# Optimization experiments

Measured on AMD Instinct MI355X. Metric: run time of the kernel, lower is better.

Reference implementation:

```python
import jax, jax.numpy as jnp
import numpy as np

DIM_X, DIM_Z, D_MODEL, N_HEADS, BATCH = 512, 256, 256, 8, 32


def sinusoidal_pe(seq_len, d_model):
    # standard sinusoidal table, rows indexed by position
    pos = np.arange(seq_len)[:, None].astype(np.float32)
    div = np.exp(np.arange(0, d_model, 2).astype(np.float32) * (-np.log(10000.0) / d_model))
    pe = np.zeros((seq_len, d_model), dtype=np.float32)
    pe[:, 0::2] = np.sin(pos * div)
    pe[:, 1::2] = np.cos(pos * div)
    return jnp.asarray(pe)


def setup_inputs() -> dict:
    key = jax.random.key(0)
    ks = jax.random.split(key, 5)
    state = jax.random.normal(ks[0], (BATCH, D_MODEL, DIM_X), dtype=jnp.float32)
    obs = jax.random.normal(ks[1], (BATCH, D_MODEL, DIM_Z), dtype=jnp.float32)
    Qp = jax.random.uniform(ks[2], (DIM_X, D_MODEL), dtype=jnp.float32)  # torch.rand init
    Wq = jax.random.normal(ks[3], (D_MODEL, D_MODEL), dtype=jnp.float32) / np.sqrt(D_MODEL)
    Wk = jax.random.normal(ks[4], (D_MODEL, D_MODEL), dtype=jnp.float32) / np.sqrt(D_MODEL)
    bq = jnp.zeros((D_MODEL,), dtype=jnp.float32)
    bk = jnp.zeros((D_MODEL,), dtype=jnp.float32)
    return {"state": state, "obs": obs, "Qp": Qp, "Wq": Wq, "bq": bq, "Wk": Wk, "bk": bk}


def reference(state, obs, Qp, Wq, bq, Wk, bk):
    bs, en, dim_x = state.shape
    dim_z = obs.shape[2]
    d_model = Qp.shape[1]
    h = N_HEADS
    hd = d_model // h
    S = dim_x + dim_z

    # mean-center over the ensemble axis
    A = state - jnp.mean(state, axis=1, keepdims=True)   # [bs, en, dim_x]
    Y = obs - jnp.mean(obs, axis=1, keepdims=True)       # [bs, en, dim_z]
    A = jnp.transpose(A, (2, 0, 1))                      # [dim_x, bs, en]
    Y = jnp.transpose(Y, (2, 0, 1))                      # [dim_z, bs, en]

    # positional encoding: batch_first=True quirk -> PE indexed along axis 1 (the bs axis)
    pe = sinusoidal_pe(bs, d_model)[None, :, :]          # [1, bs, d_model]
    query = Qp[:, None, :] + pe                          # [dim_x, bs, d_model] (broadcast of repeat)
    xy = jnp.concatenate([A, Y], axis=0) + pe            # [S, bs, d_model]

    # multi-head attention weights (V / out-proj do not affect returned quantities)
    q = (query @ Wq.T + bq).reshape(dim_x, bs, h, hd)
    k = (xy @ Wk.T + bk).reshape(S, bs, h, hd)
    scores = jnp.einsum('lbhd,sbhd->bhls', q, k) / np.sqrt(hd)  # [bs, h, dim_x, S]

    # fixed structured mask: eye(dim_x) | bottom-padded eye(dim_z)
    p1 = jnp.eye(dim_x, dtype=bool)
    p2 = jnp.concatenate([jnp.zeros((dim_x - dim_z, dim_z), dtype=bool),
                          jnp.eye(dim_z, dtype=bool)], axis=0)
    allow = jnp.concatenate([p1, p2], axis=1)            # [dim_x, S]
    scores = jnp.where(allow[None, None], scores, -jnp.inf)
    atten = jnp.mean(jax.nn.softmax(scores, axis=-1), axis=1)  # average over heads -> [bs, dim_x, S]

    # weighted merge of the ORIGINAL (uncentered) state/obs
    merge = jnp.concatenate([jnp.transpose(state, (0, 2, 1)),
                             jnp.transpose(obs, (0, 2, 1))], axis=1)  # [bs, S, en]
    new_state = jnp.einsum('bls,bse->ble', atten, merge)              # [bs, dim_x, en]
    new_state = jnp.transpose(new_state, (0, 2, 1))                   # [bs, en, dim_x]
    return new_state, atten
```

## Files before the change

### kernel.cpp

```cpp
#include <hip/hip_runtime.h>
#include <stdint.h>
#include <math.h>


#define WS_P    0
#define WS_QWT  8192
#define WS_PQ   73728
#define WS_U    81920
#define WS_V    606208
#define WS_QPT  671744
#define WS_WQT  737280

__global__ void __launch_bounds__(256)
k_tr(const float* __restrict__ Qp, const float* __restrict__ Wq,
     float* __restrict__ ws) {
  __shared__ float tile[32][33];
  int bid = blockIdx.x, t = threadIdx.x;
  const float* src; float* dst; int ti;
  if (bid < 64) { src = Qp + 65536; dst = ws + WS_QPT; ti = bid; }
  else          { src = Wq;         dst = ws + WS_WQT; ti = bid - 64; }
  int tr = ti >> 3, tc = ti & 7;
  int c = t & 31, r0 = t >> 5;
  #pragma unroll
  for (int k = 0; k < 4; ++k) {
    int r = r0 + (k << 3);
    tile[r][c] = src[(size_t)(tr * 32 + r) * 256 + tc * 32 + c];
  }
  __syncthreads();
  #pragma unroll
  for (int k = 0; k < 4; ++k) {
    int r = r0 + (k << 3);
    dst[(size_t)(tc * 32 + r) * 256 + tr * 32 + c] = tile[c][r];
  }
}

__global__ void __launch_bounds__(256)
k_pro(const float* __restrict__ Wq, float* __restrict__ ws) {
  int bid = blockIdx.x, t = threadIdx.x;
  __shared__ float lvec[256];
  const float* __restrict__ GT; float* dst;
  if (bid < 256) {
    int d = bid;
    lvec[t] = Wq[(size_t)d * 256 + t];
    GT = ws + WS_QPT; dst = ws + WS_QWT + d * 256;
  } else {
    int b = bid - 256;
    int k2 = t & ~1;
    float div = expf((float)k2 * (-9.210340371976184f / 256.f));
    float a = (float)b * div;
    lvec[t] = (t & 1) ? cosf(a) : sinf(a);
    GT = ws + WS_WQT; dst = ws + WS_PQ + b * 256;
  }
  __syncthreads();
  float acc = 0.f;
  #pragma unroll 8
  for (int e = 0; e < 256; ++e)
    acc += lvec[e] * GT[(e << 8) + t];
  dst[t] = acc;
}

__global__ void __launch_bounds__(256)
k_uv(const float* __restrict__ Wk, const float* __restrict__ bq,
     float* __restrict__ ws) {
  int bid = blockIdx.x, t = threadIdx.x;
  if (bid < 2048) {
    int h = bid >> 8, e = bid & 255;
    float acc = 0.f;
#pragma unroll 8
    for (int dd = 0; dd < 32; ++dd) {
      int d = h * 32 + dd;
      acc += ws[WS_QWT + d * 256 + t] * Wk[(size_t)d * 256 + e];
    }
    ws[WS_U + ((h << 8) + e) * 256 + t] = acc;
  } else {
    int idx = bid - 2048, b = idx >> 3, h = idx & 7;
    float acc = 0.f;
#pragma unroll 8
    for (int dd = 0; dd < 32; ++dd) {
      int d = h * 32 + dd;
      acc += (ws[WS_PQ + b * 256 + d] + bq[d]) * Wk[(size_t)d * 256 + t];
    }
    ws[WS_V + ((b << 3) + h) * 256 + t] = acc;
  }
}

__global__ void __launch_bounds__(256)
k_delta(const float* __restrict__ state, const float* __restrict__ obs,
        float* __restrict__ ws) {
  int b = blockIdx.x >> 3, jt = (blockIdx.x & 7) << 5;
  int t = threadIdx.x;
  __shared__ float Xs[256][33];
  __shared__ float Vs[2048];
  __shared__ float pd[8][8][32];
  __shared__ float pw[8][8][32];
  __shared__ float px[8][32];
  {
    int es = t >> 3, jq = t & 7;
    const float* sp = state + (size_t)b * 131072 + 256 + jt + (jq << 2);
    const float* op = obs   + (size_t)b * 65536  + jt + (jq << 2);
    #pragma unroll
    for (int k = 0; k < 8; ++k) {
      int e = es + (k << 5);
      float4 s4 = *(const float4*)(sp + (size_t)e * 512);
      float4 o4 = *(const float4*)(op + (size_t)e * 256);
      float* xr = &Xs[e][jq << 2];
      xr[0] = s4.x - o4.x; xr[1] = s4.y - o4.y;
      xr[2] = s4.z - o4.z; xr[3] = s4.w - o4.w;
    }
    for (int i = t; i < 2048; i += 256) Vs[i] = ws[WS_V + (b << 11) + i];
  }
  __syncthreads();
  int j = t & 31, eg = t >> 5, e0 = eg << 5;
  {
    float ax = 0.f;
    #pragma unroll
    for (int ei = 0; ei < 32; ++ei) ax += Xs[e0 + ei][j];
    px[eg][j] = ax;
  }
  const float* __restrict__ Ub = ws + WS_U + jt + j;
  #pragma unroll
  for (int h = 0; h < 8; ++h) {
    float dacc = 0.f, wacc = 0.f;
    const float* __restrict__ Uh = Ub + (h << 16) + (e0 << 8);
    const float* __restrict__ Vh = Vs + (h << 8) + e0;
    #pragma unroll 16
    for (int ei = 0; ei < 32; ++ei) {
      float w = Uh[ei << 8] + Vh[ei];
      dacc += Xs[e0 + ei][j] * w;
      wacc += w;
    }
    pd[eg][h][j] = dacc;
    pw[eg][h][j] = wacc;
  }
  __syncthreads();
  int h2 = t >> 5, j2 = t & 31;
  float D = 0.f, W = 0.f, X = 0.f;
  #pragma unroll
  for (int g = 0; g < 8; ++g) {
    D += pd[g][h2][j2];
    W += pw[g][h2][j2];
    X += px[g][j2];
  }
  float delta = D - X * (1.f / 256.f) * W;
  float sig = 1.f / (1.f + __expf(-delta * 0.17677669529663687f));
  __syncthreads();
  px[h2][j2] = sig;
  __syncthreads();
  if (t < 32) {
    float acc = 0.f;
    #pragma unroll
    for (int h = 0; h < 8; ++h) acc += px[h][t];
    ws[WS_P + (b << 8) + jt + t] = acc;
  }
}

__global__ void __launch_bounds__(256)
k_out(const float* __restrict__ state, const float* __restrict__ obs,
      const float* __restrict__ ws, float* __restrict__ out) {
  int bid = blockIdx.x, t = threadIdx.x;
  if (bid < 4096) {
    int row = (bid << 1) | (t >> 7);
    int tt = t & 127;
    int b = row >> 8;
    float4 sv = ((const float4*)(state + (size_t)row * 512))[tt];
    float4* wrow = (float4*)(out + (size_t)row * 512);
    if (tt < 64) {
      wrow[tt] = sv;
    } else {
      float4 ov = ((const float4*)(obs + (size_t)row * 256))[tt - 64];
      float4 p4 = ((const float4*)(ws + WS_P + b * 256))[tt - 64];
      p4.x *= 0.125f; p4.y *= 0.125f; p4.z *= 0.125f; p4.w *= 0.125f;
      float4 r;
      r.x = p4.x * sv.x + (1.f - p4.x) * ov.x;
      r.y = p4.y * sv.y + (1.f - p4.y) * ov.y;
      r.z = p4.z * sv.z + (1.f - p4.z) * ov.z;
      r.w = p4.w * sv.w + (1.f - p4.w) * ov.w;
      wrow[tt] = r;
    }
  } else {
    int g4 = (bid - 4096) * 256 + t;
    int r = g4 / 192, c = g4 - r * 192;
    int b = r >> 9, l = r & 511;
    int s0 = c << 2;
    float v[4] = {0.f, 0.f, 0.f, 0.f};
    if (l < 256) {
      if (l >= s0 && l < s0 + 4) v[l - s0] = 1.0f;
    } else {
      float p = ws[WS_P + b * 256 + (l - 256)] * 0.125f;
      if (l >= s0 && l < s0 + 4) v[l - s0] = p;
      int s2 = l + 256;
      if (s2 >= s0 && s2 < s0 + 4) v[s2 - s0] = 1.0f - p;
    }
    float4 val; val.x = v[0]; val.y = v[1]; val.z = v[2]; val.w = v[3];
    ((float4*)(out + 4194304))[g4] = val;
  }
}

extern "C" void kernel_launch(void* const* d_in, const int* in_sizes, int n_in,
                              void* d_out, int out_size, void* d_ws, size_t ws_size,
                              hipStream_t stream) {
  const float *state = nullptr, *obs = nullptr, *Qp = nullptr;
  const float *Wq = nullptr, *Wk = nullptr, *bq = nullptr, *bk = nullptr;
  for (int i = 0; i < n_in; ++i) {
    int s = in_sizes[i];
    const float* p = (const float*)d_in[i];
    if      (s == 4194304) state = p;
    else if (s == 2097152) obs = p;
    else if (s == 131072)  Qp = p;
    else if (s == 65536)   { if (!Wq) Wq = p; else Wk = p; }
    else if (s == 256)     { if (!bq) bq = p; else bk = p; }
  }
  (void)bk;
  float* out = (float*)d_out;
  float* ws  = (float*)d_ws;

  k_tr   <<<128,   256, 0, stream>>>(Qp, Wq, ws);
  k_pro  <<<288,   256, 0, stream>>>(Wq, ws);
  k_uv   <<<2304,  256, 0, stream>>>(Wk, bq, ws);
  k_delta<<<256,   256, 0, stream>>>(state, obs, ws);
  k_out  <<<16384, 256, 0, stream>>>(state, obs, ws, out);
}
```

Measured before the change: 131.2 us.

## Reassociate weight products per head and merge prologue into two kernels

Replaces the three prologue kernels (transpose, Qp·Wq / PE·Wq, then ·Wk) with two. The first transposes Qp and forms the per-head product T_h = Wq_h^T·Wk_h plus a bias term. The second multiplies Qp by T to get U and the positional encoding by T to get V. This drops one launch, removes the large Wq transpose and QWT buffer, and register-blocks the inner products. The cost is a different summation order, more flops in the Qp·T step (256-long dot per element), and an extra transposed copy of T written to the workspace.

After: 139.4 us. 6.3% more time.

```diff
diff --git a/kernel.cpp b/kernel.cpp
--- a/kernel.cpp
+++ b/kernel.cpp
@@ -4,82 +4,112 @@
 
 
 #define WS_P    0
-#define WS_QWT  8192
-#define WS_PQ   73728
 #define WS_U    81920
 #define WS_V    606208
 #define WS_QPT  671744
-#define WS_WQT  737280
-
-__global__ void __launch_bounds__(256)
-k_tr(const float* __restrict__ Qp, const float* __restrict__ Wq,
-     float* __restrict__ ws) {
-  __shared__ float tile[32][33];
+#define WS_T    737280
+#define WS_TT   1261568
+#define WS_TB   1785856
+
+__global__ void __launch_bounds__(256)
+k_A(const float* __restrict__ Qp, const float* __restrict__ Wq,
+    const float* __restrict__ Wk, const float* __restrict__ bq,
+    float* __restrict__ ws) {
   int bid = blockIdx.x, t = threadIdx.x;
-  const float* src; float* dst; int ti;
-  if (bid < 64) { src = Qp + 65536; dst = ws + WS_QPT; ti = bid; }
-  else          { src = Wq;         dst = ws + WS_WQT; ti = bid - 64; }
-  int tr = ti >> 3, tc = ti & 7;
-  int c = t & 31, r0 = t >> 5;
-  #pragma unroll
-  for (int k = 0; k < 4; ++k) {
-    int r = r0 + (k << 3);
-    tile[r][c] = src[(size_t)(tr * 32 + r) * 256 + tc * 32 + c];
-  }
-  __syncthreads();
-  #pragma unroll
-  for (int k = 0; k < 4; ++k) {
-    int r = r0 + (k << 3);
-    dst[(size_t)(tc * 32 + r) * 256 + tr * 32 + c] = tile[c][r];
-  }
-}
-
-__global__ void __launch_bounds__(256)
-k_pro(const float* __restrict__ Wq, float* __restrict__ ws) {
+  if (bid < 64) {
+    __shared__ float tile[32][33];
+    int tr = bid >> 3, tc = bid & 7;
+    int c = t & 31, r0 = t >> 5;
+    #pragma unroll
+    for (int k = 0; k < 4; ++k) {
+      int r = r0 + (k << 3);
+      tile[r][c] = Qp[65536 + (size_t)(tr * 32 + r) * 256 + tc * 32 + c];
+    }
+    __syncthreads();
+    #pragma unroll
+    for (int k = 0; k < 4; ++k) {
+      int r = r0 + (k << 3);
+      ws[WS_QPT + (size_t)(tc * 32 + r) * 256 + tr * 32 + c] = tile[c][r];
+    }
+  } else {
+    int idx = bid - 64;
+    int h = idx >> 4, e0 = (idx & 15) << 4;
+    __shared__ float wk_s[32][17];
+    __shared__ float bq_s[32];
+    {
+      int d = t >> 4, i = t & 15;
+      wk_s[d][i]      = Wk[(size_t)(h * 32 + d) * 256 + e0 + i];
+      wk_s[d + 16][i] = Wk[(size_t)(h * 32 + d + 16) * 256 + e0 + i];
+      if (t < 32) bq_s[t] = bq[h * 32 + t];
+    }
+    __syncthreads();
+    float acc[16];
+    #pragma unroll
+    for (int i = 0; i < 16; ++i) acc[i] = 0.f;
+    const float* __restrict__ wqp = Wq + (size_t)h * 8192 + t;
+    #pragma unroll 4
+    for (int d = 0; d < 32; ++d) {
+      float wq = wqp[d << 8];
+      #pragma unroll
+      for (int i = 0; i < 16; ++i) acc[i] += wk_s[d][i] * wq;
+    }
+    float* Th  = ws + WS_T  + (h << 16);
+    float* Tth = ws + WS_TT + (h << 16);
+    #pragma unroll
+    for (int i = 0; i < 16; ++i)
+      Th[(size_t)(e0 + i) * 256 + t] = acc[i];
+    #pragma unroll
+    for (int k = 0; k < 4; ++k) {
+      float4 v; v.x = acc[4*k]; v.y = acc[4*k+1]; v.z = acc[4*k+2]; v.w = acc[4*k+3];
+      *(float4*)(Tth + (size_t)t * 256 + e0 + 4 * k) = v;
+    }
+    if (t < 16) {
+      float tb = 0.f;
+      #pragma unroll
+      for (int d = 0; d < 32; ++d) tb += bq_s[d] * wk_s[d][t];
+      ws[WS_TB + h * 256 + e0 + t] = tb;
+    }
+  }
+}
+
+__global__ void __launch_bounds__(256)
+k_B(float* __restrict__ ws) {
   int bid = blockIdx.x, t = threadIdx.x;
-  __shared__ float lvec[256];
-  const float* __restrict__ GT; float* dst;
   if (bid < 256) {
-    int d = bid;
-    lvec[t] = Wq[(size_t)d * 256 + t];
-    GT = ws + WS_QPT; dst = ws + WS_QWT + d * 256;
+    int h = bid >> 5, e0 = (bid & 31) << 3;
+    __shared__ float Ts[8][256];
+    const float* __restrict__ Th = ws + WS_T + (h << 16) + (size_t)e0 * 256;
+    #pragma unroll
+    for (int i = 0; i < 8; ++i) Ts[i][t] = Th[(size_t)i * 256 + t];
+    __syncthreads();
+    float acc[8];
+    #pragma unroll
+    for (int i = 0; i < 8; ++i) acc[i] = 0.f;
+    const float* __restrict__ QT = ws + WS_QPT + t;
+    #pragma unroll 4
+    for (int c = 0; c < 256; ++c) {
+      float q = QT[c << 8];
+      #pragma unroll
+      for (int i = 0; i < 8; ++i) acc[i] += Ts[i][c] * q;
+    }
+    float* Uh = ws + WS_U + (h << 16) + (size_t)e0 * 256;
+    #pragma unroll
+    for (int i = 0; i < 8; ++i) Uh[(size_t)i * 256 + t] = acc[i];
   } else {
-    int b = bid - 256;
-    int k2 = t & ~1;
-    float div = expf((float)k2 * (-9.210340371976184f / 256.f));
-    float a = (float)b * div;
-    lvec[t] = (t & 1) ? cosf(a) : sinf(a);
-    GT = ws + WS_WQT; dst = ws + WS_PQ + b * 256;
-  }
-  __syncthreads();
-  float acc = 0.f;
-  #pragma unroll 8
-  for (int e = 0; e < 256; ++e)
-    acc += lvec[e] * GT[(e << 8) + t];
-  dst[t] = acc;
-}
-
-__global__ void __launch_bounds__(256)
-k_uv(const float* __restrict__ Wk, const float* __restrict__ bq,
-     float* __restrict__ ws) {
-  int bid = blockIdx.x, t = threadIdx.x;
-  if (bid < 2048) {
-    int h = bid >> 8, e = bid & 255;
-    float acc = 0.f;
-#pragma unroll 8
-    for (int dd = 0; dd < 32; ++dd) {
-      int d = h * 32 + dd;
-      acc += ws[WS_QWT + d * 256 + t] * Wk[(size_t)d * 256 + e];
-    }
-    ws[WS_U + ((h << 8) + e) * 256 + t] = acc;
-  } else {
-    int idx = bid - 2048, b = idx >> 3, h = idx & 7;
-    float acc = 0.f;
-#pragma unroll 8
-    for (int dd = 0; dd < 32; ++dd) {
-      int d = h * 32 + dd;
-      acc += (ws[WS_PQ + b * 256 + d] + bq[d]) * Wk[(size_t)d * 256 + t];
-    }
+    int idx = bid - 256, b = idx >> 3, h = idx & 7;
+    __shared__ float pe_s[256];
+    {
+      int k2 = t & ~1;
+      float div = expf((float)k2 * (-9.210340371976184f / 256.f));
+      float a = (float)b * div;
+      pe_s[t] = (t & 1) ? cosf(a) : sinf(a);
+    }
+    __syncthreads();
+    float acc = ws[WS_TB + h * 256 + t];
+    const float* __restrict__ Tth = ws + WS_TT + (h << 16) + t;
+    #pragma unroll 16
+    for (int c = 0; c < 256; ++c)
+      acc += pe_s[c] * Tth[c << 8];
     ws[WS_V + ((b << 3) + h) * 256 + t] = acc;
   }
 }
@@ -214,9 +244,8 @@
   float* out = (float*)d_out;
   float* ws  = (float*)d_ws;
 
-  k_tr   <<<128,   256, 0, stream>>>(Qp, Wq, ws);
-  k_pro  <<<288,   256, 0, stream>>>(Wq, ws);
-  k_uv   <<<2304,  256, 0, stream>>>(Wk, bq, ws);
+  k_A    <<<192,   256, 0, stream>>>(Qp, Wq, Wk, bq, ws);
+  k_B    <<<512,   256, 0, stream>>>(ws);
   k_delta<<<256,   256, 0, stream>>>(state, obs, ws);
   k_out  <<<16384, 256, 0, stream>>>(state, obs, ws, out);
 }
```
